# Performance work log

Hardware: AMD Instinct MI355X
Metric: run time of the kernel (lower is better)

The kernel has to match this reference:

```python
import jax, jax.numpy as jnp
import numpy as np

B, T, C, H = 16, 2048, 1024, 64

def setup_inputs() -> dict:
    key = jax.random.key(0)
    kx, kq, kk, kv = jax.random.split(key, 4)
    x = jax.random.normal(kx, (B, T, C), dtype=jnp.float32)
    Wq = jax.random.normal(kq, (C, H), dtype=jnp.float32) * (C ** -0.5)
    Wk = jax.random.normal(kk, (C, H), dtype=jnp.float32) * (C ** -0.5)
    Wv = jax.random.normal(kv, (C, H), dtype=jnp.float32) * (C ** -0.5)
    return {"x": x, "Wq": Wq, "Wk": Wk, "Wv": Wv}

def reference(x, Wq, Wk, Wv):
    # single causal self-attention head; dropout p=0.0 (identity)
    Tlen = x.shape[1]
    q = jnp.einsum('btc,ch->bth', x, Wq)  # [B,T,H]
    k = jnp.einsum('btc,ch->bth', x, Wk)
    v = jnp.einsum('btc,ch->bth', x, Wv)
    scale = q.shape[-1] ** -0.5
    scores = jnp.einsum('bth,bsh->bts', q, k) * scale  # [B,T,T]
    causal = jnp.tril(jnp.ones((Tlen, Tlen), dtype=bool))
    scores = jnp.where(causal, scores, -jnp.inf)
    weights = jax.nn.softmax(scores, axis=-1)
    out = jnp.einsum('bts,bsh->bth', weights, v)  # [B,T,H]
    return out
```

## Files before the change

### kernel.cpp

```cpp
#include <hip/hip_runtime.h>


typedef float  floatx4 __attribute__((ext_vector_type(4)));
typedef __bf16 bf16x8  __attribute__((ext_vector_type(8)));
typedef short  short8v __attribute__((ext_vector_type(8)));
typedef unsigned short ushort4v __attribute__((ext_vector_type(4)));

constexpr int Bn = 16;
constexpr int Tn = 2048;
constexpr int Cn = 1024;
constexpr int Hn = 64;
constexpr int BT = Bn * Tn;

#define QSCALE 0.1803368867f

__device__ __forceinline__ unsigned short f2b(float f) {
  unsigned int u = __builtin_bit_cast(unsigned int, f);
  u += 0x7fffu + ((u >> 16) & 1u);
  return (unsigned short)(u >> 16);
}

__device__ __forceinline__ bf16x8 cvt8(floatx4 a, floatx4 b) {
  short8v p;
  p[0] = (short)f2b(a[0]); p[1] = (short)f2b(a[1]);
  p[2] = (short)f2b(a[2]); p[3] = (short)f2b(a[3]);
  p[4] = (short)f2b(b[0]); p[5] = (short)f2b(b[1]);
  p[6] = (short)f2b(b[2]); p[7] = (short)f2b(b[3]);
  return __builtin_bit_cast(bf16x8, p);
}

__global__ __launch_bounds__(256) void pack_w(const float* __restrict__ Wq,
                                              const float* __restrict__ Wk,
                                              const float* __restrict__ Wv,
                                              unsigned short* __restrict__ Wp) {
  int gid = blockIdx.x * 256 + threadIdx.x;
  int mat = gid >> 16;
  int rem = gid & 65535;
  int k   = rem >> 6;
  int col = rem & 63;
  const float* W = (mat == 0) ? Wq : (mat == 1) ? Wk : Wv;
  float v = W[rem];
  int kb = k >> 3, j = k & 7, ct = (mat << 2) | (col >> 4), c = col & 15;
  size_t idx = ((((size_t)ct * 128) + kb) * 16 + c) * 8 + j;
  Wp[idx] = f2b(v);
}

__global__ __launch_bounds__(64) void proj_kernel(
    const float* __restrict__ x, const unsigned short* __restrict__ Wp,
    unsigned short* __restrict__ Q, unsigned short* __restrict__ K,
    unsigned short* __restrict__ Vt) {
  const int lane = threadIdx.x;
  const int quad = lane >> 4;
  const int l16  = lane & 15;
  const int rbase = blockIdx.x * 32;

  floatx4 acc[2][12];
#pragma unroll
  for (int a = 0; a < 2; ++a)
#pragma unroll
    for (int t = 0; t < 12; ++t) acc[a][t] = (floatx4){0.f, 0.f, 0.f, 0.f};

  const float* xr0 = x + (size_t)(rbase + l16) * Cn + quad * 8;
  const float* xr1 = x + (size_t)(rbase + 16 + l16) * Cn + quad * 8;

  floatx4 a00 = *reinterpret_cast<const floatx4*>(xr0);
  floatx4 a01 = *reinterpret_cast<const floatx4*>(xr0 + 4);
  floatx4 a10 = *reinterpret_cast<const floatx4*>(xr1);
  floatx4 a11 = *reinterpret_cast<const floatx4*>(xr1 + 4);

  for (int s = 0; s < 32; ++s) {
    bf16x8 af0 = cvt8(a00, a01);
    bf16x8 af1 = cvt8(a10, a11);

    if (s < 31) {
      const int koff = (s + 1) * 32;
      a00 = *reinterpret_cast<const floatx4*>(xr0 + koff);
      a01 = *reinterpret_cast<const floatx4*>(xr0 + koff + 4);
      a10 = *reinterpret_cast<const floatx4*>(xr1 + koff);
      a11 = *reinterpret_cast<const floatx4*>(xr1 + koff + 4);
    }

    const unsigned short* wb = Wp + (size_t)(s * 4 + quad) * 128 + l16 * 8;
#pragma unroll
    for (int t = 0; t < 12; ++t) {
      bf16x8 bfr = *reinterpret_cast<const bf16x8*>(wb + t * 16384);
      acc[0][t] = __builtin_amdgcn_mfma_f32_16x16x32_bf16(af0, bfr, acc[0][t], 0, 0, 0);
      acc[1][t] = __builtin_amdgcn_mfma_f32_16x16x32_bf16(af1, bfr, acc[1][t], 0, 0, 0);
    }
  }

  const int b  = rbase >> 11;
  const int tb = rbase & 2047;
#pragma unroll
  for (int rt = 0; rt < 2; ++rt) {
    const int rowloc = rt * 16 + quad * 4;
#pragma unroll
    for (int ct = 0; ct < 12; ++ct) {
      if (ct < 4) {
#pragma unroll
        for (int r = 0; r < 4; ++r)
          Q[(size_t)(rbase + rowloc + r) * Hn + ct * 16 + l16] =
              f2b(acc[rt][ct][r] * QSCALE);
      } else if (ct < 8) {
#pragma unroll
        for (int r = 0; r < 4; ++r)
          K[(size_t)(rbase + rowloc + r) * Hn + (ct - 4) * 16 + l16] =
              f2b(acc[rt][ct][r]);
      } else {
        const int h = (ct - 8) * 16 + l16;
        ushort4v v;
#pragma unroll
        for (int r = 0; r < 4; ++r) v[r] = f2b(acc[rt][ct][r]);
        *reinterpret_cast<ushort4v*>(
            &Vt[((size_t)b * Hn + h) * Tn + tb + rowloc]) = v;
      }
    }
  }
}

__global__ __launch_bounds__(256) void flash_kernel(
    const unsigned short* __restrict__ Q, const unsigned short* __restrict__ K,
    const unsigned short* __restrict__ Vt, float* __restrict__ out) {
  __shared__ alignas(16) unsigned short P[4][16][72];
  __shared__ alignas(16) float Om[4][16][68];
  __shared__ float Ll[4][16];

  const int tid  = threadIdx.x;
  const int wave = tid >> 6;
  const int lane = tid & 63;
  const int quad = lane >> 4;
  const int l16  = lane & 15;

  const int b   = blockIdx.x & 15;
  const int p16 = 127 - (blockIdx.x >> 4);
  const int qbase = p16 * 16;
  const int n_tiles  = (p16 >> 2) + 1;
  const int lastTile = p16 >> 2;
  const size_t bbase  = (size_t)b * Tn * Hn;
  const size_t vtbase = (size_t)b * Hn * Tn;

  bf16x8 qf[2];
#pragma unroll
  for (int i = 0; i < 2; ++i)
    qf[i] = *reinterpret_cast<const bf16x8*>(
        &Q[bbase + (size_t)(qbase + l16) * Hn + i * 32 + quad * 8]);

  floatx4 O[4];
#pragma unroll
  for (int i = 0; i < 4; ++i) O[i] = (floatx4){0.f, 0.f, 0.f, 0.f};
  float l_r[4] = {0.f, 0.f, 0.f, 0.f};

  for (int kt = wave; kt < n_tiles; kt += 4) {
    const int kvbase = kt * 64;

    floatx4 S[4];
#pragma unroll
    for (int ct = 0; ct < 4; ++ct) {
      floatx4 s = (floatx4){0.f, 0.f, 0.f, 0.f};
#pragma unroll
      for (int kk = 0; kk < 2; ++kk) {
        bf16x8 bfr = *reinterpret_cast<const bf16x8*>(
            &K[bbase + (size_t)(kvbase + ct * 16 + l16) * Hn + kk * 32 + quad * 8]);
        s = __builtin_amdgcn_mfma_f32_16x16x32_bf16(qf[kk], bfr, s, 0, 0, 0);
      }
      S[ct] = s;
    }

    bf16x8 vf[4][2];
#pragma unroll
    for (int ht = 0; ht < 4; ++ht)
#pragma unroll
      for (int kk = 0; kk < 2; ++kk)
        vf[ht][kk] = *reinterpret_cast<const bf16x8*>(
            &Vt[vtbase + (size_t)(ht * 16 + l16) * Tn + kvbase + kk * 32 + quad * 8]);

    if (kt == lastTile) {
#pragma unroll
      for (int ct = 0; ct < 4; ++ct)
#pragma unroll
        for (int r = 0; r < 4; ++r) {
          int trow = qbase + quad * 4 + r;
          int scol = kvbase + ct * 16 + l16;
          if (scol > trow) S[ct][r] = -1e30f;
        }
    }

#pragma unroll
    for (int r = 0; r < 4; ++r) {
      float p0 = __builtin_amdgcn_exp2f(S[0][r]);
      float p1 = __builtin_amdgcn_exp2f(S[1][r]);
      float p2 = __builtin_amdgcn_exp2f(S[2][r]);
      float p3 = __builtin_amdgcn_exp2f(S[3][r]);
      l_r[r] += (p0 + p1) + (p2 + p3);
      P[wave][quad * 4 + r][l16]      = f2b(p0);
      P[wave][quad * 4 + r][16 + l16] = f2b(p1);
      P[wave][quad * 4 + r][32 + l16] = f2b(p2);
      P[wave][quad * 4 + r][48 + l16] = f2b(p3);
    }

    bf16x8 pf0 = *reinterpret_cast<const bf16x8*>(&P[wave][l16][quad * 8]);
    bf16x8 pf1 = *reinterpret_cast<const bf16x8*>(&P[wave][l16][32 + quad * 8]);
#pragma unroll
    for (int ht = 0; ht < 4; ++ht) {
      O[ht] = __builtin_amdgcn_mfma_f32_16x16x32_bf16(pf0, vf[ht][0], O[ht], 0, 0, 0);
      O[ht] = __builtin_amdgcn_mfma_f32_16x16x32_bf16(pf1, vf[ht][1], O[ht], 0, 0, 0);
    }
  }

#pragma unroll
  for (int r = 0; r < 4; ++r)
#pragma unroll
    for (int d = 1; d < 16; d <<= 1) l_r[r] += __shfl_xor(l_r[r], d);

#pragma unroll
  for (int ht = 0; ht < 4; ++ht)
#pragma unroll
    for (int r = 0; r < 4; ++r)
      Om[wave][quad * 4 + r][ht * 16 + l16] = O[ht][r];
  if (l16 == 0) {
#pragma unroll
    for (int r = 0; r < 4; ++r) Ll[wave][quad * 4 + r] = l_r[r];
  }
  __syncthreads();

  {
    const int row = tid >> 4;
    const int c4  = (tid & 15) * 4;
    float L = (Ll[0][row] + Ll[1][row]) + (Ll[2][row] + Ll[3][row]);
    float invL = 1.0f / L;
    floatx4 o0 = *reinterpret_cast<const floatx4*>(&Om[0][row][c4]);
    floatx4 o1 = *reinterpret_cast<const floatx4*>(&Om[1][row][c4]);
    floatx4 o2 = *reinterpret_cast<const floatx4*>(&Om[2][row][c4]);
    floatx4 o3 = *reinterpret_cast<const floatx4*>(&Om[3][row][c4]);
    floatx4 res;
#pragma unroll
    for (int j = 0; j < 4; ++j)
      res[j] = ((o0[j] + o1[j]) + (o2[j] + o3[j])) * invL;
    *reinterpret_cast<floatx4*>(
        &out[bbase + (size_t)(qbase + row) * Hn + c4]) = res;
  }
}

extern "C" void kernel_launch(void* const* d_in, const int* in_sizes, int n_in,
                              void* d_out, int out_size, void* d_ws, size_t ws_size,
                              hipStream_t stream) {
  const float* x  = (const float*)d_in[0];
  const float* Wq = (const float*)d_in[1];
  const float* Wk = (const float*)d_in[2];
  const float* Wv = (const float*)d_in[3];
  float* out = (float*)d_out;

  char* ws = (char*)d_ws;
  unsigned short* Q  = (unsigned short*)(ws);
  unsigned short* Kb = (unsigned short*)(ws + ((size_t)4 << 20));
  unsigned short* Vt = (unsigned short*)(ws + ((size_t)8 << 20));
  unsigned short* Wp = (unsigned short*)(ws + ((size_t)12 << 20));

  pack_w<<<dim3(768), dim3(256), 0, stream>>>(Wq, Wk, Wv, Wp);
  proj_kernel<<<dim3(BT / 32), dim3(64), 0, stream>>>(x, Wp, Q, Kb, Vt);
  flash_kernel<<<dim3(16 * 128), dim3(256), 0, stream>>>(Q, Kb, Vt, out);
}
```

Measured before the change: 285.3 us.

## Double-buffer x loads with nontemporal hints and reorder flash block mapping

The projection kernel now prefetches x two k-steps ahead in alternating register buffers using nontemporal loads. It also batches all twelve weight-fragment loads ahead of the MFMA chain to hide memory latency. Separately, the flash kernel's block-to-(batch, query tile) mapping changes so consecutive blocks walk one batch's tiles rather than interleaving batches. That changes load balance across the heavy-first causal ordering and L2 locality, and the extra live registers could lower occupancy.

```diff
diff --git a/kernel.cpp b/kernel.cpp
--- a/kernel.cpp
+++ b/kernel.cpp
@@ -28,6 +28,8 @@
   p[6] = (short)f2b(b[2]); p[7] = (short)f2b(b[3]);
   return __builtin_bit_cast(bf16x8, p);
 }
+
+#define NTL4(p) __builtin_nontemporal_load(reinterpret_cast<const floatx4*>(p))
 
 __global__ __launch_bounds__(256) void pack_w(const float* __restrict__ Wq,
                                               const float* __restrict__ Wk,
@@ -63,29 +65,49 @@
   const float* xr0 = x + (size_t)(rbase + l16) * Cn + quad * 8;
   const float* xr1 = x + (size_t)(rbase + 16 + l16) * Cn + quad * 8;
 
-  floatx4 a00 = *reinterpret_cast<const floatx4*>(xr0);
-  floatx4 a01 = *reinterpret_cast<const floatx4*>(xr0 + 4);
-  floatx4 a10 = *reinterpret_cast<const floatx4*>(xr1);
-  floatx4 a11 = *reinterpret_cast<const floatx4*>(xr1 + 4);
-
-  for (int s = 0; s < 32; ++s) {
-    bf16x8 af0 = cvt8(a00, a01);
-    bf16x8 af1 = cvt8(a10, a11);
-
-    if (s < 31) {
-      const int koff = (s + 1) * 32;
-      a00 = *reinterpret_cast<const floatx4*>(xr0 + koff);
-      a01 = *reinterpret_cast<const floatx4*>(xr0 + koff + 4);
-      a10 = *reinterpret_cast<const floatx4*>(xr1 + koff);
-      a11 = *reinterpret_cast<const floatx4*>(xr1 + koff + 4);
-    }
-
-    const unsigned short* wb = Wp + (size_t)(s * 4 + quad) * 128 + l16 * 8;
-#pragma unroll
-    for (int t = 0; t < 12; ++t) {
-      bf16x8 bfr = *reinterpret_cast<const bf16x8*>(wb + t * 16384);
-      acc[0][t] = __builtin_amdgcn_mfma_f32_16x16x32_bf16(af0, bfr, acc[0][t], 0, 0, 0);
-      acc[1][t] = __builtin_amdgcn_mfma_f32_16x16x32_bf16(af1, bfr, acc[1][t], 0, 0, 0);
+  floatx4 e00 = NTL4(xr0),      e01 = NTL4(xr0 + 4);
+  floatx4 e10 = NTL4(xr1),      e11 = NTL4(xr1 + 4);
+  floatx4 o00 = NTL4(xr0 + 32), o01 = NTL4(xr0 + 36);
+  floatx4 o10 = NTL4(xr1 + 32), o11 = NTL4(xr1 + 36);
+
+  for (int s = 0; s < 32; s += 2) {
+    {
+      bf16x8 af0 = cvt8(e00, e01);
+      bf16x8 af1 = cvt8(e10, e11);
+      const unsigned short* wb = Wp + (size_t)(s * 4 + quad) * 128 + l16 * 8;
+      bf16x8 bfr[12];
+#pragma unroll
+      for (int t = 0; t < 12; ++t)
+        bfr[t] = *reinterpret_cast<const bf16x8*>(wb + t * 16384);
+      if (s + 2 < 32) {
+        const int ko = (s + 2) * 32;
+        e00 = NTL4(xr0 + ko); e01 = NTL4(xr0 + ko + 4);
+        e10 = NTL4(xr1 + ko); e11 = NTL4(xr1 + ko + 4);
+      }
+#pragma unroll
+      for (int t = 0; t < 12; ++t) {
+        acc[0][t] = __builtin_amdgcn_mfma_f32_16x16x32_bf16(af0, bfr[t], acc[0][t], 0, 0, 0);
+        acc[1][t] = __builtin_amdgcn_mfma_f32_16x16x32_bf16(af1, bfr[t], acc[1][t], 0, 0, 0);
+      }
+    }
+    {
+      bf16x8 af0 = cvt8(o00, o01);
+      bf16x8 af1 = cvt8(o10, o11);
+      const unsigned short* wb = Wp + (size_t)((s + 1) * 4 + quad) * 128 + l16 * 8;
+      bf16x8 bfr[12];
+#pragma unroll
+      for (int t = 0; t < 12; ++t)
+        bfr[t] = *reinterpret_cast<const bf16x8*>(wb + t * 16384);
+      if (s + 3 < 32) {
+        const int ko = (s + 3) * 32;
+        o00 = NTL4(xr0 + ko); o01 = NTL4(xr0 + ko + 4);
+        o10 = NTL4(xr1 + ko); o11 = NTL4(xr1 + ko + 4);
+      }
+#pragma unroll
+      for (int t = 0; t < 12; ++t) {
+        acc[0][t] = __builtin_amdgcn_mfma_f32_16x16x32_bf16(af0, bfr[t], acc[0][t], 0, 0, 0);
+        acc[1][t] = __builtin_amdgcn_mfma_f32_16x16x32_bf16(af1, bfr[t], acc[1][t], 0, 0, 0);
+      }
     }
   }
 
@@ -131,8 +153,8 @@
   const int quad = lane >> 4;
   const int l16  = lane & 15;
 
-  const int b   = blockIdx.x & 15;
-  const int p16 = 127 - (blockIdx.x >> 4);
+  const int b   = blockIdx.x >> 7;
+  const int p16 = 127 - (blockIdx.x & 127);
   const int qbase = p16 * 16;
   const int n_tiles  = (p16 >> 2) + 1;
   const int lastTile = p16 >> 2;
```

Result: slower. 322.0 us (+12.8%).
